# Optimization experiments

Measured on AMD Instinct MI355X. Metric: run time of the kernel, lower is better.

The kernel has to match this reference:

```python
import jax, jax.numpy as jnp
import numpy as np

DIM = 1024
NUM_HEADS = 16
DIM_HEAD = 64
INNER = NUM_HEADS * DIM_HEAD  # 1024
B, N = 2, 2048


def setup_inputs() -> dict:
    key = jax.random.key(0)
    k1, k2, k3 = jax.random.split(key, 3)
    x = jax.random.normal(k1, (B, N, DIM), dtype=jnp.float32)
    # nn.Linear(dim, inner*3, bias=False): weight [3*inner, dim]; y = x @ W^T
    w_qkv = jax.random.normal(k2, (3 * INNER, DIM), dtype=jnp.float32) * (DIM ** -0.5)
    # to_out: Linear(inner, dim) with bias
    w_out = jax.random.normal(k3, (DIM, INNER), dtype=jnp.float32) * (INNER ** -0.5)
    b_out = jnp.zeros((DIM,), dtype=jnp.float32)
    return {"x": x, "w_qkv": w_qkv, "w_out": w_out, "b_out": b_out}


def reference(x, w_qkv, w_out, b_out):
    b, n, d = x.shape
    scale = DIM_HEAD ** -0.5
    qkv = jnp.einsum('bnd,ed->bne', x, w_qkv)  # [b, n, 3*inner]
    q, k, v = jnp.split(qkv, 3, axis=-1)
    # [b, n, h, dh] -> [b, h, n, dh]
    reshape = lambda t: t.reshape(b, n, NUM_HEADS, DIM_HEAD).transpose(0, 2, 1, 3)
    q, k, v = reshape(q), reshape(k), reshape(v)
    dots = jnp.einsum('bhqd,bhkd->bhqk', q, k) * scale  # [b, h, n, n]
    attn = jax.nn.softmax(dots, axis=-1)
    out = jnp.einsum('bhqk,bhkd->bhqd', attn, v)
    out = out.transpose(0, 2, 1, 3).reshape(b, n, INNER)
    out = jnp.einsum('bni,oi->bno', out, w_out) + b_out
    return out
```

## Files before the change

kernel.cpp:

```cpp
#include <hip/hip_runtime.h>
#include <hip/hip_bf16.h>
#include <stdint.h>

typedef unsigned short u16;
typedef short bf16x8 __attribute__((ext_vector_type(8)));
typedef float f32x4 __attribute__((ext_vector_type(4)));
typedef float f32x16 __attribute__((ext_vector_type(16)));
typedef u16 u16x4 __attribute__((ext_vector_type(4)));
typedef unsigned int uint2v __attribute__((ext_vector_type(2)));

#define DIMX  1024
#define NHEAD 16
#define DH    64
#define INNER 1024
#define BATCH 2
#define SEQ   2048
#define MTOT  (BATCH*SEQ)
#define EQKV  (3*INNER)

__device__ __forceinline__ u16 f2bf(float f) {
  unsigned int x = __float_as_uint(f);
  unsigned int r = (x + 0x7FFFu + ((x >> 16) & 1u)) >> 16;
  return (u16)r;
}

__device__ __forceinline__ unsigned int cvtpk(float lo, float hi) {
  unsigned int r;
  asm("v_cvt_pk_bf16_f32 %0, %1, %2" : "=v"(r) : "v"(lo), "v"(hi));
  return r;
}

__device__ __forceinline__ void plswap_u(unsigned int& x, unsigned int& y) {
  auto r = __builtin_amdgcn_permlane32_swap(x, y, false, false);
  x = r[0]; y = r[1];
}
__device__ __forceinline__ void plswap_f2(float v, float& a, float& b) {
  unsigned int x = __float_as_uint(v), y = __float_as_uint(v);
  auto r = __builtin_amdgcn_permlane32_swap(x, y, false, false);
  a = __uint_as_float(r[0]); b = __uint_as_float(r[1]);
}

__device__ __forceinline__ void async16(void* lds, const void* g) {
  __builtin_amdgcn_global_load_lds(
      (const __attribute__((address_space(1))) unsigned int*)g,
      (__attribute__((address_space(3))) unsigned int*)lds,
      16, 0, 0);
}

__device__ __forceinline__ int swz4(int r) { return (r ^ (r >> 2)) & 3; }

__global__ void cvt_kernel(const float* __restrict__ in, u16* __restrict__ out, int n4) {
  int i = blockIdx.x * blockDim.x + threadIdx.x;
  if (i < n4) {
    float4 v = ((const float4*)in)[i];
    u16x4 o;
    o[0] = f2bf(v.x); o[1] = f2bf(v.y); o[2] = f2bf(v.z); o[3] = f2bf(v.w);
    ((u16x4*)out)[i] = o;
  }
}

__global__ __launch_bounds__(256) void gemm_qkv(const u16* __restrict__ X, const u16* __restrict__ W,
                                                u16* __restrict__ Qo, u16* __restrict__ Ko,
                                                u16* __restrict__ Vt) {
  __shared__ short sAll[16384];
  short* sA = sAll;
  short* sB = sAll + 8192;
  const int tid = threadIdx.x;
  const int wv = tid >> 6, l = tid & 63;
  const int lo = l & 15, hi = l >> 4;
  const int wr = wv >> 1, wc = wv & 1;

  int lin = blockIdx.x;
  int wgid = (lin & 7) * 96 + (lin >> 3);
  const int bx = wgid / 32;
  const int by = wgid % 32;
  const int tn = bx * 128, tm = by * 128;

  f32x4 acc[4][4];
#pragma unroll
  for (int i = 0; i < 4; i++)
#pragma unroll
    for (int j = 0; j < 4; j++) acc[i][j] = (f32x4){0.f, 0.f, 0.f, 0.f};

  auto stage = [&](int buf, int kt) {
    int k0 = kt * 32;
    int off = buf * 4096;
#pragma unroll
    for (int c = 0; c < 2; c++) {
      int R0 = wv * 32 + c * 16;
      int r = R0 + (l >> 2);
      int sc = ((l & 3) ^ swz4(r)) * 8;
      async16(&sA[off + R0 * 32], &X[(size_t)(tm + r) * DIMX + k0 + sc]);
      async16(&sB[off + R0 * 32], &W[(size_t)(tn + r) * DIMX + k0 + sc]);
    }
  };

  stage(0, 0);
  __syncthreads();

  for (int kt = 0; kt < DIMX / 32; kt++) {
    const int buf = kt & 1;
    if (kt + 1 < DIMX / 32) stage(buf ^ 1, kt + 1);
    bf16x8 af[4], bf[4];
#pragma unroll
    for (int i = 0; i < 4; i++) {
      int r = wr * 64 + i * 16 + lo;
      af[i] = *(const bf16x8*)&sA[buf * 4096 + r * 32 + ((hi ^ swz4(r)) * 8)];
    }
#pragma unroll
    for (int j = 0; j < 4; j++) {
      int r = wc * 64 + j * 16 + lo;
      bf[j] = *(const bf16x8*)&sB[buf * 4096 + r * 32 + ((hi ^ swz4(r)) * 8)];
    }
#pragma unroll
    for (int i = 0; i < 4; i++)
#pragma unroll
      for (int j = 0; j < 4; j++)
        acc[i][j] = __builtin_amdgcn_mfma_f32_16x16x32_bf16(af[i], bf[j], acc[i][j], 0, 0, 0);
    __syncthreads();
  }

  const int cls = tn >> 10;
  const float scale = 0.125f * 1.44269504088896f;

  if (cls < 2) {
#pragma unroll
    for (int i = 0; i < 4; i++) {
      int mbase = tm + wr * 64 + i * 16 + hi * 4;
#pragma unroll
      for (int j = 0; j < 4; j++) {
        int e = tn + wc * 64 + j * 16 + lo;
        int e2 = e & 1023, h = e2 >> 6, d = e2 & 63;
#pragma unroll
        for (int r = 0; r < 4; r++) {
          int mm = mbase + r;
          int b = mm >> 11, n = mm & 2047;
          float v = acc[i][j][r];
          if (cls == 0)
            Qo[(((size_t)(b * NHEAD + h)) * SEQ + n) * DH + d] = f2bf(v * scale);
          else
            Ko[(((size_t)(b * NHEAD + h)) * SEQ + n) * DH + d] = f2bf(v);
        }
      }
    }
  } else {
#pragma unroll
    for (int i = 0; i < 4; i++) {
#pragma unroll
      for (int j = 0; j < 4; j++) {
        int e = wc * 64 + j * 16 + lo;
#pragma unroll
        for (int r = 0; r < 4; r++) {
          int n = wr * 64 + i * 16 + hi * 4 + r;
          sAll[e * 128 + (((n >> 3) ^ (e & 15)) * 8) + (n & 7)] = (short)f2bf(acc[i][j][r]);
        }
      }
    }
    __syncthreads();
    int er = tid >> 1, half = tid & 1;
    int e2 = tn + er - 2048;
    int h = e2 >> 6, d = e2 & 63;
    int b = tm >> 11, nb = tm & 2047;
    u16* dst = &Vt[(((size_t)(b * NHEAD + h)) * DH + d) * SEQ + nb + half * 64];
#pragma unroll
    for (int k = 0; k < 8; k++) {
      int phys = (half * 8 + k) ^ (er & 15);
      bf16x8 v = *(const bf16x8*)&sAll[er * 128 + phys * 8];
      *(bf16x8*)&dst[k * 8] = v;
    }
  }
}

__global__ __launch_bounds__(256) void attn_kernel(const u16* __restrict__ Q, const u16* __restrict__ Kd,
                                                   const u16* __restrict__ Vt, u16* __restrict__ O) {
  __shared__ short sK[2][64 * 64];
  __shared__ short sV[2][64 * 64];
  const int tid = threadIdx.x, wv = tid >> 6, l = tid & 63;
  const int l31 = l & 31, hi5 = l >> 5, l7 = l & 7;

  int lin = blockIdx.y * gridDim.x + blockIdx.x;
  int wgid = (lin & 7) * 64 + (lin >> 3);
  int bx = wgid & 15;
  int bh = wgid >> 4;

  const int qw = bx * 128 + wv * 32;
  const u16* Qb = Q + (size_t)bh * SEQ * DH;
  const u16* Kb = Kd + (size_t)bh * SEQ * DH;
  const u16* Vb = Vt + (size_t)bh * DH * SEQ;

  bf16x8 qf[4];
#pragma unroll
  for (int kd = 0; kd < 4; kd++)
    qf[kd] = *(const bf16x8*)&Qb[(size_t)(qw + l31) * DH + kd * 16 + hi5 * 8];

  f32x16 o0, o1;
#pragma unroll
  for (int r = 0; r < 16; r++) { o0[r] = 0.f; o1[r] = 0.f; }
  float lsum = 0.f;
  const float CSHIFT = 12.0f;

  auto stage = [&](int buf, int t) {
    int kv0 = t * 64;
#pragma unroll
    for (int c = 0; c < 2; c++) {
      int rbase = wv * 16 + c * 8;
      int gr = rbase + (l >> 3);
      int sc = ((l & 7) ^ (l >> 3)) * 8;
      async16(&sK[buf][rbase * 64], &Kb[(size_t)(kv0 + gr) * DH + sc]);
      async16(&sV[buf][rbase * 64], &Vb[(size_t)gr * SEQ + kv0 + sc]);
    }
  };

  stage(0, 0);
  __syncthreads();

  for (int t = 0; t < SEQ / 64; t++) {
    const int cur = t & 1;
    if (t + 1 < SEQ / 64) stage(cur ^ 1, t + 1);

    bf16x8 kf0[4], kf1[4], vf0[4], vf1[4];
#pragma unroll
    for (int kd = 0; kd < 4; kd++) {
      int c16 = ((kd * 2 + hi5) ^ l7) * 8;
      kf0[kd] = *(const bf16x8*)&sK[cur][l31 * 64 + c16];
      kf1[kd] = *(const bf16x8*)&sK[cur][(32 + l31) * 64 + c16];
      vf0[kd] = *(const bf16x8*)&sV[cur][l31 * 64 + c16];
      vf1[kd] = *(const bf16x8*)&sV[cur][(32 + l31) * 64 + c16];
    }

    f32x16 s0, s1;
#pragma unroll
    for (int r = 0; r < 16; r++) { s0[r] = -CSHIFT; s1[r] = -CSHIFT; }
#pragma unroll
    for (int kd = 0; kd < 4; kd++) {
      s0 = __builtin_amdgcn_mfma_f32_32x32x16_bf16(kf0[kd], qf[kd], s0, 0, 0, 0);
      s1 = __builtin_amdgcn_mfma_f32_32x32x16_bf16(kf1[kd], qf[kd], s1, 0, 0, 0);
    }

    float sm[16];
#pragma unroll
    for (int r = 0; r < 16; r++) {
      s0[r] = __builtin_amdgcn_exp2f(s0[r]);
      s1[r] = __builtin_amdgcn_exp2f(s1[r]);
      sm[r] = s0[r] + s1[r];
    }
#pragma unroll
    for (int st = 8; st > 0; st >>= 1)
#pragma unroll
      for (int r = 0; r < st; r++) sm[r] += sm[r + st];
    lsum += sm[0];

    bf16x8 pa[4];
#pragma unroll
    for (int ks = 0; ks < 4; ks++) {
      const int sft = (ks & 1) * 8;
      float e0 = (ks < 2) ? s0[sft + 0] : s1[sft + 0];
      float e1 = (ks < 2) ? s0[sft + 1] : s1[sft + 1];
      float e2 = (ks < 2) ? s0[sft + 2] : s1[sft + 2];
      float e3 = (ks < 2) ? s0[sft + 3] : s1[sft + 3];
      float e4 = (ks < 2) ? s0[sft + 4] : s1[sft + 4];
      float e5 = (ks < 2) ? s0[sft + 5] : s1[sft + 5];
      float e6 = (ks < 2) ? s0[sft + 6] : s1[sft + 6];
      float e7 = (ks < 2) ? s0[sft + 7] : s1[sft + 7];
      unsigned int w0 = cvtpk(e0, e1);
      unsigned int w1 = cvtpk(e2, e3);
      unsigned int w2 = cvtpk(e4, e5);
      unsigned int w3 = cvtpk(e6, e7);
      plswap_u(w0, w2);
      plswap_u(w1, w3);
      union { unsigned int w[4]; bf16x8 v; } u;
      u.w[0] = w0; u.w[1] = w1; u.w[2] = w2; u.w[3] = w3;
      pa[ks] = u.v;
    }

#pragma unroll
    for (int ks = 0; ks < 4; ks++) {
      o0 = __builtin_amdgcn_mfma_f32_32x32x16_bf16(vf0[ks], pa[ks], o0, 0, 0, 0);
      o1 = __builtin_amdgcn_mfma_f32_32x32x16_bf16(vf1[ks], pa[ks], o1, 0, 0, 0);
    }
    __syncthreads();
  }

  float la, lb;
  plswap_f2(lsum, la, lb);
  float inv = 1.0f / (la + lb);

  int b = bh >> 4, h = bh & 15;
  int q = qw + l31;
  size_t orow = ((size_t)(b * SEQ + q)) * INNER + h * 64;
#pragma unroll
  for (int half = 0; half < 2; half++) {
    const f32x16& oo = half ? o1 : o0;
#pragma unroll
    for (int g = 0; g < 4; g++) {
      uint2v pk2;
      pk2[0] = cvtpk(oo[g * 4 + 0] * inv, oo[g * 4 + 1] * inv);
      pk2[1] = cvtpk(oo[g * 4 + 2] * inv, oo[g * 4 + 3] * inv);
      int dv = half * 32 + g * 8 + 4 * hi5;
      *(uint2v*)&O[orow + dv] = pk2;
    }
  }
}

__global__ __launch_bounds__(256) void gemm_out(const u16* __restrict__ A, const u16* __restrict__ W,
                                                const float* __restrict__ bias, float* __restrict__ out) {
  __shared__ short sAll[16384];
  short* sA = sAll;
  short* sB = sAll + 8192;
  const int tid = threadIdx.x;
  const int wv = tid >> 6, l = tid & 63;
  const int lo = l & 15, hi = l >> 4;
  const int wr = wv >> 1, wc = wv & 1;

  int lin = blockIdx.x;
  int wgid = (lin & 7) * 32 + (lin >> 3);
  const int bx = wgid / 32;
  const int by = wgid % 32;
  const int tn = bx * 128, tm = by * 128;

  f32x4 acc[4][4];
#pragma unroll
  for (int i = 0; i < 4; i++)
#pragma unroll
    for (int j = 0; j < 4; j++) acc[i][j] = (f32x4){0.f, 0.f, 0.f, 0.f};

  auto stage = [&](int buf, int kt) {
    int k0 = kt * 32;
    int off = buf * 4096;
#pragma unroll
    for (int c = 0; c < 2; c++) {
      int R0 = wv * 32 + c * 16;
      int r = R0 + (l >> 2);
      int sc = ((l & 3) ^ swz4(r)) * 8;
      async16(&sA[off + R0 * 32], &A[(size_t)(tm + r) * INNER + k0 + sc]);
      async16(&sB[off + R0 * 32], &W[(size_t)(tn + r) * INNER + k0 + sc]);
    }
  };

  stage(0, 0);
  __syncthreads();

  for (int kt = 0; kt < INNER / 32; kt++) {
    const int buf = kt & 1;
    if (kt + 1 < INNER / 32) stage(buf ^ 1, kt + 1);
    bf16x8 af[4], bf[4];
#pragma unroll
    for (int i = 0; i < 4; i++) {
      int r = wr * 64 + i * 16 + lo;
      af[i] = *(const bf16x8*)&sA[buf * 4096 + r * 32 + ((hi ^ swz4(r)) * 8)];
    }
#pragma unroll
    for (int j = 0; j < 4; j++) {
      int r = wc * 64 + j * 16 + lo;
      bf[j] = *(const bf16x8*)&sB[buf * 4096 + r * 32 + ((hi ^ swz4(r)) * 8)];
    }
#pragma unroll
    for (int i = 0; i < 4; i++)
#pragma unroll
      for (int j = 0; j < 4; j++)
        acc[i][j] = __builtin_amdgcn_mfma_f32_16x16x32_bf16(af[i], bf[j], acc[i][j], 0, 0, 0);
    __syncthreads();
  }

#pragma unroll
  for (int i = 0; i < 4; i++) {
    int mbase = tm + wr * 64 + i * 16 + hi * 4;
#pragma unroll
    for (int j = 0; j < 4; j++) {
      int col = tn + wc * 64 + j * 16 + lo;
      float bv = bias[col];
#pragma unroll
      for (int r = 0; r < 4; r++)
        out[(size_t)(mbase + r) * DIMX + col] = acc[i][j][r] + bv;
    }
  }
}

extern "C" void kernel_launch(void* const* d_in, const int* in_sizes, int n_in,
                              void* d_out, int out_size, void* d_ws, size_t ws_size,
                              hipStream_t stream) {
  const float* x     = (const float*)d_in[0];
  const float* w_qkv = (const float*)d_in[1];
  const float* w_out = (const float*)d_in[2];
  const float* b_out = (const float*)d_in[3];

  char* ws = (char*)d_ws;
  u16* xb    = (u16*)(ws);
  u16* wqkvb = (u16*)(ws + (size_t)8  * (1<<20));
  u16* woutb = (u16*)(ws + (size_t)14 * (1<<20));
  u16* Qd    = (u16*)(ws + (size_t)16 * (1<<20));
  u16* Kdd   = (u16*)(ws + (size_t)24 * (1<<20));
  u16* Vtd   = (u16*)(ws + (size_t)32 * (1<<20));
  u16* Od    = (u16*)(ws + (size_t)40 * (1<<20));

  cvt_kernel<<<(MTOT * DIMX / 4 + 255) / 256, 256, 0, stream>>>(x, xb, MTOT * DIMX / 4);
  cvt_kernel<<<(EQKV * DIMX / 4 + 255) / 256, 256, 0, stream>>>(w_qkv, wqkvb, EQKV * DIMX / 4);
  cvt_kernel<<<(DIMX * INNER / 4 + 255) / 256, 256, 0, stream>>>(w_out, woutb, DIMX * INNER / 4);

  gemm_qkv<<<768, 256, 0, stream>>>(xb, wqkvb, Qd, Kdd, Vtd);
  attn_kernel<<<dim3(SEQ / 128, BATCH * NHEAD), 256, 0, stream>>>(Qd, Kdd, Vtd, Od);
  gemm_out<<<256, 256, 0, stream>>>(Od, woutb, b_out, (float*)d_out);
}
```

Before: 129.3 us.

## Double KV tile to 128 per barrier and merge the three convert kernels

The attention kernel now stages 128 keys/values per pipeline step instead of 64, processing two 64-wide sub-blocks per iteration. This halves the number of __syncthreads barriers and staging rounds, using a new 16-way XOR swizzle for the wider V tile. The three fp32-to-bf16 conversion launches are fused into one kernel that picks its source by index, removing two launches. The cost is doubled LDS (64 KB per block), which may reduce occupancy.

```diff
diff --git a/kernel.cpp b/kernel.cpp
--- a/kernel.cpp
+++ b/kernel.cpp
@@ -17,6 +17,7 @@
 #define SEQ   2048
 #define MTOT  (BATCH*SEQ)
 #define EQKV  (3*INNER)
+#define KVB   128
 
 __device__ __forceinline__ u16 f2bf(float f) {
   unsigned int x = __float_as_uint(f);
@@ -49,14 +50,21 @@
 
 __device__ __forceinline__ int swz4(int r) { return (r ^ (r >> 2)) & 3; }
 
-__global__ void cvt_kernel(const float* __restrict__ in, u16* __restrict__ out, int n4) {
+#define X4C (MTOT * DIMX / 4)
+#define W4C (EQKV * DIMX / 4)
+#define O4C (DIMX * INNER / 4)
+__global__ void cvt_all(const float* __restrict__ x, const float* __restrict__ wq,
+                        const float* __restrict__ wo, u16* __restrict__ xb,
+                        u16* __restrict__ wqb, u16* __restrict__ wob) {
   int i = blockIdx.x * blockDim.x + threadIdx.x;
-  if (i < n4) {
-    float4 v = ((const float4*)in)[i];
-    u16x4 o;
-    o[0] = f2bf(v.x); o[1] = f2bf(v.y); o[2] = f2bf(v.z); o[3] = f2bf(v.w);
-    ((u16x4*)out)[i] = o;
-  }
+  const float* src; u16* dst; int off;
+  if (i < X4C)            { src = x;  dst = xb;  off = i; }
+  else if (i < X4C + W4C) { src = wq; dst = wqb; off = i - X4C; }
+  else                    { src = wo; dst = wob; off = i - X4C - W4C; }
+  float4 v = ((const float4*)src)[off];
+  u16x4 o;
+  o[0] = f2bf(v.x); o[1] = f2bf(v.y); o[2] = f2bf(v.z); o[3] = f2bf(v.w);
+  ((u16x4*)dst)[off] = o;
 }
 
 __global__ __launch_bounds__(256) void gemm_qkv(const u16* __restrict__ X, const u16* __restrict__ W,
@@ -173,10 +181,11 @@
 
 __global__ __launch_bounds__(256) void attn_kernel(const u16* __restrict__ Q, const u16* __restrict__ Kd,
                                                    const u16* __restrict__ Vt, u16* __restrict__ O) {
-  __shared__ short sK[2][64 * 64];
-  __shared__ short sV[2][64 * 64];
+  __shared__ short sK[2][KVB * 64];
+  __shared__ short sV[2][64 * KVB];
   const int tid = threadIdx.x, wv = tid >> 6, l = tid & 63;
   const int l31 = l & 31, hi5 = l >> 5, l7 = l & 7;
+  const int l15 = l31 & 15;
 
   int lin = blockIdx.y * gridDim.x + blockIdx.x;
   int wgid = (lin & 7) * 64 + (lin >> 3);
@@ -200,83 +209,90 @@
   const float CSHIFT = 12.0f;
 
   auto stage = [&](int buf, int t) {
-    int kv0 = t * 64;
-#pragma unroll
-    for (int c = 0; c < 2; c++) {
-      int rbase = wv * 16 + c * 8;
-      int gr = rbase + (l >> 3);
-      int sc = ((l & 7) ^ (l >> 3)) * 8;
-      async16(&sK[buf][rbase * 64], &Kb[(size_t)(kv0 + gr) * DH + sc]);
-      async16(&sV[buf][rbase * 64], &Vb[(size_t)gr * SEQ + kv0 + sc]);
+    int kv0 = t * KVB;
+#pragma unroll
+    for (int c = 0; c < 4; c++) {
+      int rbK = wv * 32 + c * 8;
+      int grK = rbK + (l >> 3);
+      int scK = ((l & 7) ^ (grK & 7)) * 8;
+      async16(&sK[buf][rbK * 64], &Kb[(size_t)(kv0 + grK) * DH + scK]);
+      int rbV = wv * 16 + c * 4;
+      int grV = rbV + (l >> 4);
+      int scV = ((l & 15) ^ (grV & 15)) * 8;
+      async16(&sV[buf][rbV * KVB], &Vb[(size_t)grV * SEQ + kv0 + scV]);
     }
   };
 
   stage(0, 0);
   __syncthreads();
 
-  for (int t = 0; t < SEQ / 64; t++) {
+  for (int t = 0; t < SEQ / KVB; t++) {
     const int cur = t & 1;
-    if (t + 1 < SEQ / 64) stage(cur ^ 1, t + 1);
-
-    bf16x8 kf0[4], kf1[4], vf0[4], vf1[4];
-#pragma unroll
-    for (int kd = 0; kd < 4; kd++) {
-      int c16 = ((kd * 2 + hi5) ^ l7) * 8;
-      kf0[kd] = *(const bf16x8*)&sK[cur][l31 * 64 + c16];
-      kf1[kd] = *(const bf16x8*)&sK[cur][(32 + l31) * 64 + c16];
-      vf0[kd] = *(const bf16x8*)&sV[cur][l31 * 64 + c16];
-      vf1[kd] = *(const bf16x8*)&sV[cur][(32 + l31) * 64 + c16];
-    }
-
-    f32x16 s0, s1;
-#pragma unroll
-    for (int r = 0; r < 16; r++) { s0[r] = -CSHIFT; s1[r] = -CSHIFT; }
-#pragma unroll
-    for (int kd = 0; kd < 4; kd++) {
-      s0 = __builtin_amdgcn_mfma_f32_32x32x16_bf16(kf0[kd], qf[kd], s0, 0, 0, 0);
-      s1 = __builtin_amdgcn_mfma_f32_32x32x16_bf16(kf1[kd], qf[kd], s1, 0, 0, 0);
-    }
-
-    float sm[16];
-#pragma unroll
-    for (int r = 0; r < 16; r++) {
-      s0[r] = __builtin_amdgcn_exp2f(s0[r]);
-      s1[r] = __builtin_amdgcn_exp2f(s1[r]);
-      sm[r] = s0[r] + s1[r];
-    }
-#pragma unroll
-    for (int st = 8; st > 0; st >>= 1)
-#pragma unroll
-      for (int r = 0; r < st; r++) sm[r] += sm[r + st];
-    lsum += sm[0];
-
-    bf16x8 pa[4];
-#pragma unroll
-    for (int ks = 0; ks < 4; ks++) {
-      const int sft = (ks & 1) * 8;
-      float e0 = (ks < 2) ? s0[sft + 0] : s1[sft + 0];
-      float e1 = (ks < 2) ? s0[sft + 1] : s1[sft + 1];
-      float e2 = (ks < 2) ? s0[sft + 2] : s1[sft + 2];
-      float e3 = (ks < 2) ? s0[sft + 3] : s1[sft + 3];
-      float e4 = (ks < 2) ? s0[sft + 4] : s1[sft + 4];
-      float e5 = (ks < 2) ? s0[sft + 5] : s1[sft + 5];
-      float e6 = (ks < 2) ? s0[sft + 6] : s1[sft + 6];
-      float e7 = (ks < 2) ? s0[sft + 7] : s1[sft + 7];
-      unsigned int w0 = cvtpk(e0, e1);
-      unsigned int w1 = cvtpk(e2, e3);
-      unsigned int w2 = cvtpk(e4, e5);
-      unsigned int w3 = cvtpk(e6, e7);
-      plswap_u(w0, w2);
-      plswap_u(w1, w3);
-      union { unsigned int w[4]; bf16x8 v; } u;
-      u.w[0] = w0; u.w[1] = w1; u.w[2] = w2; u.w[3] = w3;
-      pa[ks] = u.v;
-    }
-
-#pragma unroll
-    for (int ks = 0; ks < 4; ks++) {
-      o0 = __builtin_amdgcn_mfma_f32_32x32x16_bf16(vf0[ks], pa[ks], o0, 0, 0, 0);
-      o1 = __builtin_amdgcn_mfma_f32_32x32x16_bf16(vf1[ks], pa[ks], o1, 0, 0, 0);
+    if (t + 1 < SEQ / KVB) stage(cur ^ 1, t + 1);
+
+#pragma unroll
+    for (int hh = 0; hh < 2; hh++) {
+      bf16x8 kf0[4], kf1[4], vf0[4], vf1[4];
+#pragma unroll
+      for (int kd = 0; kd < 4; kd++) {
+        int c16 = ((kd * 2 + hi5) ^ l7) * 8;
+        kf0[kd] = *(const bf16x8*)&sK[cur][(hh * 64 + l31) * 64 + c16];
+        kf1[kd] = *(const bf16x8*)&sK[cur][(hh * 64 + 32 + l31) * 64 + c16];
+        int uV = ((hh * 8 + kd * 2 + hi5) ^ l15) * 8;
+        vf0[kd] = *(const bf16x8*)&sV[cur][l31 * KVB + uV];
+        vf1[kd] = *(const bf16x8*)&sV[cur][(32 + l31) * KVB + uV];
+      }
+
+      f32x16 s0, s1;
+#pragma unroll
+      for (int r = 0; r < 16; r++) { s0[r] = -CSHIFT; s1[r] = -CSHIFT; }
+#pragma unroll
+      for (int kd = 0; kd < 4; kd++) {
+        s0 = __builtin_amdgcn_mfma_f32_32x32x16_bf16(kf0[kd], qf[kd], s0, 0, 0, 0);
+        s1 = __builtin_amdgcn_mfma_f32_32x32x16_bf16(kf1[kd], qf[kd], s1, 0, 0, 0);
+      }
+
+      float sm[16];
+#pragma unroll
+      for (int r = 0; r < 16; r++) {
+        s0[r] = __builtin_amdgcn_exp2f(s0[r]);
+        s1[r] = __builtin_amdgcn_exp2f(s1[r]);
+        sm[r] = s0[r] + s1[r];
+      }
+#pragma unroll
+      for (int st = 8; st > 0; st >>= 1)
+#pragma unroll
+        for (int r = 0; r < st; r++) sm[r] += sm[r + st];
+      lsum += sm[0];
+
+      bf16x8 pa[4];
+#pragma unroll
+      for (int ks = 0; ks < 4; ks++) {
+        const int sft = (ks & 1) * 8;
+        float e0 = (ks < 2) ? s0[sft + 0] : s1[sft + 0];
+        float e1 = (ks < 2) ? s0[sft + 1] : s1[sft + 1];
+        float e2 = (ks < 2) ? s0[sft + 2] : s1[sft + 2];
+        float e3 = (ks < 2) ? s0[sft + 3] : s1[sft + 3];
+        float e4 = (ks < 2) ? s0[sft + 4] : s1[sft + 4];
+        float e5 = (ks < 2) ? s0[sft + 5] : s1[sft + 5];
+        float e6 = (ks < 2) ? s0[sft + 6] : s1[sft + 6];
+        float e7 = (ks < 2) ? s0[sft + 7] : s1[sft + 7];
+        unsigned int w0 = cvtpk(e0, e1);
+        unsigned int w1 = cvtpk(e2, e3);
+        unsigned int w2 = cvtpk(e4, e5);
+        unsigned int w3 = cvtpk(e6, e7);
+        plswap_u(w0, w2);
+        plswap_u(w1, w3);
+        union { unsigned int w[4]; bf16x8 v; } u;
+        u.w[0] = w0; u.w[1] = w1; u.w[2] = w2; u.w[3] = w3;
+        pa[ks] = u.v;
+      }
+
+#pragma unroll
+      for (int ks = 0; ks < 4; ks++) {
+        o0 = __builtin_amdgcn_mfma_f32_32x32x16_bf16(vf0[ks], pa[ks], o0, 0, 0, 0);
+        o1 = __builtin_amdgcn_mfma_f32_32x32x16_bf16(vf1[ks], pa[ks], o1, 0, 0, 0);
+      }
     }
     __syncthreads();
   }
@@ -393,9 +409,7 @@
   u16* Vtd   = (u16*)(ws + (size_t)32 * (1<<20));
   u16* Od    = (u16*)(ws + (size_t)40 * (1<<20));
 
-  cvt_kernel<<<(MTOT * DIMX / 4 + 255) / 256, 256, 0, stream>>>(x, xb, MTOT * DIMX / 4);
-  cvt_kernel<<<(EQKV * DIMX / 4 + 255) / 256, 256, 0, stream>>>(w_qkv, wqkvb, EQKV * DIMX / 4);
-  cvt_kernel<<<(DIMX * INNER / 4 + 255) / 256, 256, 0, stream>>>(w_out, woutb, DIMX * INNER / 4);
+  cvt_all<<<(X4C + W4C + O4C) / 256, 256, 0, stream>>>(x, w_qkv, w_out, xb, wqkvb, woutb);
 
   gemm_qkv<<<768, 256, 0, stream>>>(xb, wqkvb, Qd, Kdd, Vtd);
   attn_kernel<<<dim3(SEQ / 128, BATCH * NHEAD), 256, 0, stream>>>(Qd, Kdd, Vtd, Od);
```

Measured after the change: 140.2 us. +8.4%, slower.
